# Kernel tuning notes

Measured on AMD Instinct MI355X. Metric: run time of the kernel, lower is better.

The kernel has to match this reference:

```python
import jax, jax.numpy as jnp
import numpy as np

B, C, M = 1024, 64, 512  # batch, cluster_dim, num_clusters


def setup_inputs() -> dict:
    key = jax.random.key(0)
    k1, k2, k3 = jax.random.split(key, 3)
    x = jax.random.normal(k1, (B, C, M), dtype=jnp.float32)
    running_mean = jax.random.normal(k2, (1, C, M), dtype=jnp.float32) * 0.1
    # per-cluster whitening subspaces: identity + small symmetric perturbation
    A = jax.random.normal(k3, (M, C, C), dtype=jnp.float32) * 0.05
    subspaces = jnp.eye(C, dtype=jnp.float32)[None] + 0.5 * (A + jnp.swapaxes(A, -1, -2))
    return {"x": x, "running_mean": running_mean, "subspaces": subspaces}


def reference(x, running_mean, subspaces):
    # ZCANormSVDPI inference forward:
    #   x: (B, C, M); running_mean: (1, C, M); subspaces: (M, C, C)
    #   xc = x - running_mean; per-cluster m: z[m] = subspaces[m] @ xc[:, :, m]^T
    #   output permuted back to (B, C, M)
    xc = x - running_mean                      # (B, C, M)
    z = jnp.einsum('mcd,bdm->bcm', subspaces, xc)  # (B, C, M)
    return z
```

## Files before the change

kernel.cpp:

```cpp
#include <hip/hip_runtime.h>


typedef __attribute__((ext_vector_type(8))) short short8;
typedef __attribute__((ext_vector_type(4))) float f32x4;

namespace {
constexpr int Mm = 512, Cc = 64, Bb = 1024;
constexpr int MT = 8;
constexpr int BT = 16;
constexpr int NB = 8;
constexpr int ZP = 12;
constexpr size_t LDSB = 128 * 128 + 1024 * ZP * 4;

__device__ __forceinline__ unsigned short f2bf(float v) {
  unsigned uu = __float_as_uint(v);
  uu = (uu + 0x7fffu + ((uu >> 16) & 1u)) >> 16;
  return (unsigned short)uu;
}
__device__ __forceinline__ unsigned pack2(float a, float b) {
  return (unsigned)f2bf(a) | ((unsigned)f2bf(b) << 16);
}
}

#define ELEM(V, I) \
  ((I) == 0 ? (V).x : (I) == 1 ? (V).y : (I) == 2 ? (V).z : (V).w)

__global__ __launch_bounds__(512, 4) void zca_v7(
    const float* __restrict__ x, const float* __restrict__ mean,
    const float* __restrict__ S, float* __restrict__ out) {
  extern __shared__ unsigned char lds[];
  unsigned char* xl = lds;
  float* zl = (float*)(lds + 16384);

  const int tid = threadIdx.x;
  const int l = tid & 63;
  const int w = __builtin_amdgcn_readfirstlane(tid >> 6);

  const int id = blockIdx.x;
  const int sw = ((id & 7) << 6) + (id >> 3);
  const int m0 = (sw >> 3) * MT;
  const int b0 = (sw & 7) * (BT * NB);

  const int mq = l & 1;
  const int e = l >> 1;
  const int g2 = w >> 1;

#define ISSUE(ST, T)                                                         \
  {                                                                          \
    _Pragma("unroll") for (int dd = 0; dd < 2; ++dd)                         \
        _Pragma("unroll") for (int p = 0; p < 2; ++p)                        \
            ST[dd * 2 + p] = *(const float4*)(                               \
                x + (size_t)((b0 + (T)*BT + p * 8 + w) * Cc + 2 * e + dd) *  \
                        Mm + m0 + mq * 4);                                   \
  }

#define STAGE(ST)                                                            \
  {                                                                          \
    _Pragma("unroll") for (int p = 0; p < 2; ++p) {                          \
      _Pragma("unroll") for (int i = 0; i < 4; ++i) {                        \
        const int row = (mq * 4 + i) * BT + p * 8 + w;                       \
        const unsigned v = pack2(ELEM(ST[p], i) - ELEM(mvE, i),              \
                                 ELEM(ST[2 + p], i) - ELEM(mvO, i));         \
        *(unsigned*)(xl + row * 128 + (((e >> 2) ^ w) << 4) +                \
                     ((e & 3) << 2)) = v;                                    \
      }                                                                      \
    }                                                                        \
  }

#define BAR()                                          \
  {                                                    \
    asm volatile("s_waitcnt lgkmcnt(0)" ::: "memory"); \
    __builtin_amdgcn_s_barrier();                      \
  }

  float4 st0[4], st1[4];

  ISSUE(st0, 0)
  ISSUE(st1, 1)
  const float4 mvE =
      *(const float4*)(mean + (size_t)(2 * e) * Mm + m0 + mq * 4);
  const float4 mvO =
      *(const float4*)(mean + (size_t)(2 * e + 1) * Mm + m0 + mq * 4);

  short8 A[4][2];
#pragma unroll
  for (int ct = 0; ct < 4; ++ct) {
#pragma unroll
    for (int ks = 0; ks < 2; ++ks) {
      const float* sp = S + ((size_t)(m0 + w) * Cc + ct * 16 + (l & 15)) * Cc +
                        ks * 32 + (l >> 4) * 8;
      const float4 f0 = *(const float4*)sp;
      const float4 f1 = *(const float4*)(sp + 4);
      short8 a;
      a[0] = (short)f2bf(f0.x); a[1] = (short)f2bf(f0.y);
      a[2] = (short)f2bf(f0.z); a[3] = (short)f2bf(f0.w);
      a[4] = (short)f2bf(f1.x); a[5] = (short)f2bf(f1.y);
      a[6] = (short)f2bf(f1.z); a[7] = (short)f2bf(f1.w);
      A[ct][ks] = a;
    }
  }
  STAGE(st0)
  BAR()

#define ITER(T, STC, STN)                                                      \
  {                                                                            \
    const int rb = (w * 16 + (l & 15)) * 128;                                  \
    const short8 Bf0 =                                                         \
        *(const short8*)(xl + rb + ((((l >> 4)) ^ (l & 7)) << 4));             \
    const short8 Bf1 =                                                         \
        *(const short8*)(xl + rb + (((4 | (l >> 4)) ^ (l & 7)) << 4));         \
    if ((T) + 2 < NB) ISSUE(STN, (T) + 2)                                      \
    f32x4 acc[4];                                                              \
    _Pragma("unroll") for (int ct = 0; ct < 4; ++ct) acc[ct] =                 \
        (f32x4){0.f, 0.f, 0.f, 0.f};                                          \
    _Pragma("unroll") for (int ct = 0; ct < 4; ++ct) acc[ct] =                 \
        __builtin_amdgcn_mfma_f32_16x16x32_bf16(A[ct][0], Bf0, acc[ct], 0, 0,  \
                                                0);                            \
    _Pragma("unroll") for (int ct = 0; ct < 4; ++ct) acc[ct] =                 \
        __builtin_amdgcn_mfma_f32_16x16x32_bf16(A[ct][1], Bf1, acc[ct], 0, 0,  \
                                                0);                            \
    _Pragma("unroll") for (int ct = 0; ct < 4; ++ct) {                         \
      _Pragma("unroll") for (int r = 0; r < 4; ++r) {                          \
        const int c_ = ct * 16 + (l >> 4) * 4 + r;                             \
        const int zrow = c_ * 16 + (l & 15);                                   \
        zl[zrow * ZP + (w ^ (l >> 4))] = acc[ct][r];                           \
      }                                                                        \
    }                                                                          \
    BAR()                                  \
    if ((T) + 1 < NB) STAGE(STC)                                               \
    _Pragma("unroll") for (int t2 = 0; t2 < 4; ++t2) {                         \
      const int zrow = t2 * 256 + w * 32 + e;                                  \
      float4 v = *(const float4*)(zl + zrow * ZP + mq * 4);                    \
      if (g2 & 1) {                                                            \
        float t = v.x; v.x = v.y; v.y = t;                                     \
        t = v.z; v.z = v.w; v.w = t;                                           \
      }                                                                        \
      if (g2 & 2) {                                                            \
        float t = v.x; v.x = v.z; v.z = t;                                     \
        t = v.y; v.y = v.w; v.w = t;                                           \
      }                                                                        \
      *(float4*)(out + (size_t)((b0 + (T)*BT + (zrow & 15)) * Cc +             \
                                (zrow >> 4)) * Mm + m0 + mq * 4) = v;          \
    }                                                                          \
    if ((T) < NB - 1) BAR()                    \
  }

  ITER(0, st1, st0)
  ITER(1, st0, st1)
  ITER(2, st1, st0)
  ITER(3, st0, st1)
  ITER(4, st1, st0)
  ITER(5, st0, st1)
  ITER(6, st1, st0)
  ITER(7, st0, st1)

#undef ITER
#undef BAR
#undef STAGE
#undef ISSUE
}

extern "C" void kernel_launch(void* const* d_in, const int* in_sizes, int n_in,
                              void* d_out, int out_size, void* d_ws,
                              size_t ws_size, hipStream_t stream) {
  const float* x = (const float*)d_in[0];
  const float* mean = (const float*)d_in[1];
  const float* S = (const float*)d_in[2];
  float* out = (float*)d_out;
  const int nblocks = (Mm / MT) * (Bb / (BT * NB));
  hipLaunchKernelGGL(zca_v7, dim3(nblocks), dim3(512), LDSB, stream, x, mean,
                     S, out);
}
```

Baseline: 80.93 us.

## Precompute S·mean in prep kernel and retile main GEMM kernel

After: 131.9 us. 63.0% more time.

```diff
diff --git a/kernel.cpp b/kernel.cpp
--- a/kernel.cpp
+++ b/kernel.cpp
@@ -1,4 +1,5 @@
 #include <hip/hip_runtime.h>
+#include <hip/hip_bf16.h>
 
 
 typedef __attribute__((ext_vector_type(8))) short short8;
@@ -6,64 +7,78 @@
 
 namespace {
 constexpr int Mm = 512, Cc = 64, Bb = 1024;
-constexpr int MT = 8;
-constexpr int BT = 16;
-constexpr int NB = 8;
-constexpr int ZP = 12;
-constexpr size_t LDSB = 128 * 128 + 1024 * ZP * 4;
+constexpr int MT = 16, BT = 16, NB = 4;
 
-__device__ __forceinline__ unsigned short f2bf(float v) {
-  unsigned uu = __float_as_uint(v);
-  uu = (uu + 0x7fffu + ((uu >> 16) & 1u)) >> 16;
-  return (unsigned short)uu;
-}
-__device__ __forceinline__ unsigned pack2(float a, float b) {
-  return (unsigned)f2bf(a) | ((unsigned)f2bf(b) << 16);
+__device__ __forceinline__ short bfc(float f) {
+  __hip_bfloat16 h = __float2bfloat16(f);
+  union { __hip_bfloat16 b; short s; } u;
+  u.b = h;
+  return u.s;
 }
 }
 
-#define ELEM(V, I) \
-  ((I) == 0 ? (V).x : (I) == 1 ? (V).y : (I) == 2 ? (V).z : (V).w)
+#define ELEM(V, I) ((I) == 0 ? (V).x : (I) == 1 ? (V).y : (I) == 2 ? (V).z : (V).w)
 
-__global__ __launch_bounds__(512, 4) void zca_v7(
-    const float* __restrict__ x, const float* __restrict__ mean,
-    const float* __restrict__ S, float* __restrict__ out) {
+__global__ __launch_bounds__(256) void zca_prep(const float* __restrict__ S,
+                                                const float* __restrict__ mean,
+                                                float* __restrict__ Tt) {
+  const int m = blockIdx.x;
+  const int tid = threadIdx.x;
+  const int c = tid >> 2, dq = tid & 3;
+  __shared__ float part[256];
+  const float* sp = S + (size_t)m * 4096 + c * 64 + dq * 16;
+  float acc = 0.f;
+#pragma unroll
+  for (int jj = 0; jj < 4; ++jj) {
+    const float4 sv = *(const float4*)(sp + jj * 4);
+#pragma unroll
+    for (int k = 0; k < 4; ++k)
+      acc += ELEM(sv, k) * mean[(size_t)(dq * 16 + jj * 4 + k) * Mm + m];
+  }
+  part[tid] = acc;
+  __syncthreads();
+  if (tid < 64)
+    Tt[(size_t)tid * Mm + m] =
+        part[tid * 4] + part[tid * 4 + 1] + part[tid * 4 + 2] + part[tid * 4 + 3];
+}
+
+__global__ __launch_bounds__(512, 4) void zca_v8(
+    const float* __restrict__ x, const float* __restrict__ S,
+    const float* __restrict__ Tt, float* __restrict__ out) {
   extern __shared__ unsigned char lds[];
   unsigned char* xl = lds;
-  float* zl = (float*)(lds + 16384);
+  float* zl = (float*)(lds + 32768);
 
   const int tid = threadIdx.x;
   const int l = tid & 63;
   const int w = __builtin_amdgcn_readfirstlane(tid >> 6);
 
-  const int id = blockIdx.x;
-  const int sw = ((id & 7) << 6) + (id >> 3);
-  const int m0 = (sw >> 3) * MT;
-  const int b0 = (sw & 7) * (BT * NB);
+  const int xcd = blockIdx.x & 7, ord = blockIdx.x >> 3;
+  const int m0 = (xcd * 4 + (ord & 3)) * MT;
+  const int b0 = (ord >> 2) * (BT * NB);
 
-  const int mq = l & 1;
-  const int e = l >> 1;
-  const int g2 = w >> 1;
+  const int ds8 = tid & 7, mq = (tid >> 3) & 3, bl = tid >> 5;
+  const int rrow = tid >> 2, mqr = tid & 3;
+  const int Qm = mqr ^ ((tid >> 4) & 3);
+  const int psw = (w >> 2) & 1;
 
-#define ISSUE(ST, T)                                                         \
+  float4 st[8];
+
+#define ISSUE(T)                                                             \
   {                                                                          \
-    _Pragma("unroll") for (int dd = 0; dd < 2; ++dd)                         \
-        _Pragma("unroll") for (int p = 0; p < 2; ++p)                        \
-            ST[dd * 2 + p] = *(const float4*)(                               \
-                x + (size_t)((b0 + (T)*BT + p * 8 + w) * Cc + 2 * e + dd) *  \
-                        Mm + m0 + mq * 4);                                   \
+    _Pragma("unroll") for (int j = 0; j < 8; ++j) st[j] =                    \
+        *(const float4*)(x + (size_t)((b0 + (T)*BT + bl) * Cc + ds8 * 8 + j) \
+                                 * Mm + m0 + mq * 4);                        \
   }
 
-#define STAGE(ST)                                                            \
+#define STAGE()                                                              \
   {                                                                          \
-    _Pragma("unroll") for (int p = 0; p < 2; ++p) {                          \
-      _Pragma("unroll") for (int i = 0; i < 4; ++i) {                        \
-        const int row = (mq * 4 + i) * BT + p * 8 + w;                       \
-        const unsigned v = pack2(ELEM(ST[p], i) - ELEM(mvE, i),              \
-                                 ELEM(ST[2 + p], i) - ELEM(mvO, i));         \
-        *(unsigned*)(xl + row * 128 + (((e >> 2) ^ w) << 4) +                \
-                     ((e & 3) << 2)) = v;                                    \
-      }                                                                      \
+    _Pragma("unroll") for (int i = 0; i < 4; ++i) {                          \
+      short8 v8;                                                             \
+      _Pragma("unroll") for (int j = 0; j < 8; ++j) v8[j] =                  \
+          bfc(ELEM(st[j], i));                                               \
+      *(short8*)(xl + ((mq * 4 + i) * 16 + bl) * 128 +                       \
+                 ((ds8 ^ (bl & 7)) << 4)) = v8;                              \
     }                                                                        \
   }
 
@@ -73,88 +88,92 @@
     __builtin_amdgcn_s_barrier();                      \
   }
 
-  float4 st0[4], st1[4];
+#define ZW(H)                                                                  \
+  {                                                                            \
+    _Pragma("unroll") for (int mi = 0; mi < 2; ++mi)                           \
+    _Pragma("unroll") for (int cth = 0; cth < 2; ++cth)                        \
+    _Pragma("unroll") for (int r = 0; r < 4; ++r) {                            \
+      const int mloc = w * 2 + mi, h = l >> 4, bz = l & 15;                    \
+      const int zrow = (cth * 16 + h * 4 + r) * 16 + bz;                       \
+      const int col =                                                          \
+          ((mloc & 3) ^ h) | ((((mloc >> 2) ^ (bz >> 2)) & 3) << 2);           \
+      zl[zrow * 16 + col] = acc[mi][(H)*2 + cth][r];                           \
+    }                                                                          \
+  }
 
-  ISSUE(st0, 0)
-  ISSUE(st1, 1)
-  const float4 mvE =
-      *(const float4*)(mean + (size_t)(2 * e) * Mm + m0 + mq * 4);
-  const float4 mvO =
-      *(const float4*)(mean + (size_t)(2 * e + 1) * Mm + m0 + mq * 4);
+#define ZR(H, T)                                                               \
+  {                                                                            \
+    _Pragma("unroll") for (int t2 = 0; t2 < 4; ++t2) {                         \
+      const int zrow = t2 * 128 + rrow;                                        \
+      float4 v = *(const float4*)(zl + zrow * 16 + mqr * 4);                   \
+      if (t2 & 1) {                                \
+        float tt = v.x; v.x = v.z; v.z = tt;                                   \
+        tt = v.y; v.y = v.w; v.w = tt;                                         \
+      }                                                                        \
+      if (psw) {                                   \
+        float tt = v.x; v.x = v.y; v.y = tt;                                   \
+        tt = v.z; v.z = v.w; v.w = tt;                                         \
+      }                                                                        \
+      const int cl = (H)*32 + t2 * 8 + w, bz = rrow & 15;                      \
+      const float4 tq =                                                        \
+          *(const float4*)(Tt + (size_t)cl * Mm + m0 + Qm * 4);                \
+      const float4 o =                                                         \
+          make_float4(v.x - tq.x, v.y - tq.y, v.z - tq.z, v.w - tq.w);         \
+      *(float4*)(out + (size_t)((b0 + (T)*BT + bz) * Cc + cl) * Mm + m0 +      \
+                 Qm * 4) = o;                                                  \
+    }                                                                          \
+  }
 
-  short8 A[4][2];
-#pragma unroll
-  for (int ct = 0; ct < 4; ++ct) {
-#pragma unroll
-    for (int ks = 0; ks < 2; ++ks) {
-      const float* sp = S + ((size_t)(m0 + w) * Cc + ct * 16 + (l & 15)) * Cc +
-                        ks * 32 + (l >> 4) * 8;
-      const float4 f0 = *(const float4*)sp;
-      const float4 f1 = *(const float4*)(sp + 4);
-      short8 a;
-      a[0] = (short)f2bf(f0.x); a[1] = (short)f2bf(f0.y);
-      a[2] = (short)f2bf(f0.z); a[3] = (short)f2bf(f0.w);
-      a[4] = (short)f2bf(f1.x); a[5] = (short)f2bf(f1.y);
-      a[6] = (short)f2bf(f1.z); a[7] = (short)f2bf(f1.w);
-      A[ct][ks] = a;
-    }
+#define ITER(T)                                                                \
+  {                                                                            \
+    short8 Bf[2][2];                                                           \
+    _Pragma("unroll") for (int mi = 0; mi < 2; ++mi)                           \
+    _Pragma("unroll") for (int ks = 0; ks < 2; ++ks) Bf[mi][ks] =              \
+        *(const short8*)(xl + ((w * 2 + mi) * 16 + (l & 15)) * 128 +           \
+                         (((ks * 4 + (l >> 4)) ^ (l & 7)) << 4));              \
+    f32x4 acc[2][4];                                                           \
+    _Pragma("unroll") for (int mi = 0; mi < 2; ++mi)                           \
+    _Pragma("unroll") for (int ct = 0; ct < 4; ++ct) acc[mi][ct] =             \
+        (f32x4){0.f, 0.f, 0.f, 0.f};                                           \
+    _Pragma("unroll") for (int ks = 0; ks < 2; ++ks)                           \
+    _Pragma("unroll") for (int mi = 0; mi < 2; ++mi)                           \
+    _Pragma("unroll") for (int ct = 0; ct < 4; ++ct) {                         \
+      const float* sp = S + ((size_t)(m0 + w * 2 + mi) * Cc + ct * 16 +        \
+                             (l & 15)) * Cc + ks * 32 + (l >> 4) * 8;          \
+      const float4 f0 = *(const float4*)sp;                                    \
+      const float4 f1v = *(const float4*)(sp + 4);                             \
+      short8 a;                                                                \
+      a[0] = bfc(f0.x); a[1] = bfc(f0.y); a[2] = bfc(f0.z); a[3] = bfc(f0.w);  \
+      a[4] = bfc(f1v.x); a[5] = bfc(f1v.y); a[6] = bfc(f1v.z);                 \
+      a[7] = bfc(f1v.w);                                                       \
+      acc[mi][ct] = __builtin_amdgcn_mfma_f32_16x16x32_bf16(                   \
+          a, Bf[mi][ks], acc[mi][ct], 0, 0, 0);                                \
+    }                                                                          \
+    ZW(0)                                                                      \
+    BAR()                                                                      \
+    ZR(0, T)                                                                   \
+    if ((T) < NB - 1) { STAGE() }                                              \
+    if ((T) < NB - 2) { ISSUE((T) + 2) }                                       \
+    BAR()                                                                      \
+    ZW(1)                                                                      \
+    BAR()                                                                      \
+    ZR(1, T)                                                                   \
+    if ((T) < NB - 1) BAR()                                                    \
   }
-  STAGE(st0)
+
+  ISSUE(0)
+  STAGE()
+  ISSUE(1)
   BAR()
 
-#define ITER(T, STC, STN)                                                      \
-  {                                                                            \
-    const int rb = (w * 16 + (l & 15)) * 128;                                  \
-    const short8 Bf0 =                                                         \
-        *(const short8*)(xl + rb + ((((l >> 4)) ^ (l & 7)) << 4));             \
-    const short8 Bf1 =                                                         \
-        *(const short8*)(xl + rb + (((4 | (l >> 4)) ^ (l & 7)) << 4));         \
-    if ((T) + 2 < NB) ISSUE(STN, (T) + 2)                                      \
-    f32x4 acc[4];                                                              \
-    _Pragma("unroll") for (int ct = 0; ct < 4; ++ct) acc[ct] =                 \
-        (f32x4){0.f, 0.f, 0.f, 0.f};                                          \
-    _Pragma("unroll") for (int ct = 0; ct < 4; ++ct) acc[ct] =                 \
-        __builtin_amdgcn_mfma_f32_16x16x32_bf16(A[ct][0], Bf0, acc[ct], 0, 0,  \
-                                                0);                            \
-    _Pragma("unroll") for (int ct = 0; ct < 4; ++ct) acc[ct] =                 \
-        __builtin_amdgcn_mfma_f32_16x16x32_bf16(A[ct][1], Bf1, acc[ct], 0, 0,  \
-                                                0);                            \
-    _Pragma("unroll") for (int ct = 0; ct < 4; ++ct) {                         \
-      _Pragma("unroll") for (int r = 0; r < 4; ++r) {                          \
-        const int c_ = ct * 16 + (l >> 4) * 4 + r;                             \
-        const int zrow = c_ * 16 + (l & 15);                                   \
-        zl[zrow * ZP + (w ^ (l >> 4))] = acc[ct][r];                           \
-      }                                                                        \
-    }                                                                          \
-    BAR()                                  \
-    if ((T) + 1 < NB) STAGE(STC)                                               \
-    _Pragma("unroll") for (int t2 = 0; t2 < 4; ++t2) {                         \
-      const int zrow = t2 * 256 + w * 32 + e;                                  \
-      float4 v = *(const float4*)(zl + zrow * ZP + mq * 4);                    \
-      if (g2 & 1) {                                                            \
-        float t = v.x; v.x = v.y; v.y = t;                                     \
-        t = v.z; v.z = v.w; v.w = t;                                           \
-      }                                                                        \
-      if (g2 & 2) {                                                            \
-        float t = v.x; v.x = v.z; v.z = t;                                     \
-        t = v.y; v.y = v.w; v.w = t;                                           \
-      }                                                                        \
-      *(float4*)(out + (size_t)((b0 + (T)*BT + (zrow & 15)) * Cc +             \
-                                (zrow >> 4)) * Mm + m0 + mq * 4) = v;          \
-    }                                                                          \
-    if ((T) < NB - 1) BAR()                    \
-  }
-
-  ITER(0, st1, st0)
-  ITER(1, st0, st1)
-  ITER(2, st1, st0)
-  ITER(3, st0, st1)
-  ITER(4, st1, st0)
-  ITER(5, st0, st1)
-  ITER(6, st1, st0)
-  ITER(7, st0, st1)
+  ITER(0)
+  ITER(1)
+  ITER(2)
+  ITER(3)
 
 #undef ITER
+#undef ZR
+#undef ZW
 #undef BAR
 #undef STAGE
 #undef ISSUE
@@ -167,7 +186,9 @@
   const float* mean = (const float*)d_in[1];
   const float* S = (const float*)d_in[2];
   float* out = (float*)d_out;
+  float* Tt = (float*)d_ws;
+  hipLaunchKernelGGL(zca_prep, dim3(Mm), dim3(256), 0, stream, S, mean, Tt);
   const int nblocks = (Mm / MT) * (Bb / (BT * NB));
-  hipLaunchKernelGGL(zca_v7, dim3(nblocks), dim3(512), LDSB, stream, x, mean,
-                     S, out);
+  hipLaunchKernelGGL(zca_v8, dim3(nblocks), dim3(512), 65536, stream, x, S, Tt,
+                     out);
 }
```
